# Optimization experiments

Hardware: AMD Instinct MI355X
Metric: run time of the kernel (lower is better)

Reference implementation:

```python
import jax, jax.numpy as jnp
import numpy as np

NBINS = 256  # tf.histogram_fixed_width(..., nbins=256)


def _colorspace():
    # tf.clip_by_value(tf.range(-1.0, 1.01, delta=1/127), -1, 1) -> 256 values
    cs = -1.0 + jnp.arange(NBINS, dtype=jnp.float32) / 127.0
    return jnp.clip(cs, -1.0, 1.0)


def _equalize_histogram(chan):
    # chan: (H, W) float32 in [-1, 1]
    h, w = chan.shape
    v = jnp.clip(chan.ravel(), -1.0, 1.0)
    idx = jnp.clip(((v + 1.0) * (NBINS / 2.0)).astype(jnp.int32), 0, NBINS - 1)
    hist = jnp.zeros(NBINS, jnp.int32).at[idx].add(1)
    cdf = jnp.cumsum(hist)
    cdf_min = jnp.min(cdf)
    pix_cnt = float(h * w)
    return (cdf - cdf_min).astype(jnp.float32) * 2.0 / (pix_cnt - 1.0) - 1.0


def _interpolate(dx, dy, x):
    # dx, dy: (K,) ; x: (N,) -> (N,) piecewise-linear interp via nearest-bin argmin
    delvals = jnp.abs(dx[None, :] - x[:, None])  # (N, K) big intermediate, as in TF
    ind1 = jnp.argmin(delvals, axis=1)
    ind0 = jnp.maximum(ind1 - 1, 0)
    x0, x1 = dx[ind0], dx[ind1]
    y0, y1 = dy[ind0], dy[ind1]
    denom = x1 - x0
    safe = jnp.where(denom == 0.0, 1.0, denom)  # guard flat-CDF degenerate bins
    interp = y0 + (y1 - y0) * (x - x0) / safe
    return jnp.where(x <= dx[0], dy[0], jnp.where(x >= dx[-1], dy[-1], interp))


def setup_inputs() -> dict:
    key = jax.random.key(0)
    k1, k2 = jax.random.split(key)
    H, W = 1024, 1024
    src = jax.random.uniform(k1, (H, W, 3), jnp.float32, minval=-1.0, maxval=1.0)
    tgt = jax.random.uniform(k2, (H, W, 3), jnp.float32, minval=-1.0, maxval=1.0)
    return {"src": src, "tgt": tgt}


def reference(src, tgt):
    h, w, _ = src.shape
    cs = _colorspace()
    res = []
    for i in range(3):
        s = src[:, :, i]
        t = tgt[:, :, i]
        cdfsrc = _equalize_histogram(s)
        cdftgt = _equalize_histogram(t)
        pxmap = _interpolate(cdftgt, cs, cdfsrc)      # (256,) color map
        mapped = _interpolate(cs, pxmap, s.ravel())   # (H*W,) per-pixel lookup
        res.append(mapped.reshape(h, w))
    return jnp.stack(res, axis=2)
```

## Files before the change

### kernel.cpp

```cpp
#include <hip/hip_runtime.h>

#define NBINS 256
#define SLOT (6 * NBINS)

__device__ __forceinline__ float csv(int i) {
    float c = -1.0f + (float)i / 127.0f;
    return fminf(fmaxf(c, -1.0f), 1.0f);
}

__device__ __forceinline__ int binof(float v) {
    v = fminf(fmaxf(v, -1.0f), 1.0f);
    int b = (int)((v + 1.0f) * 128.0f);
    return min(max(b, 0), NBINS - 1);
}

__global__ __launch_bounds__(256) void hm_hist(const float* __restrict__ src,
                                               const float* __restrict__ tgt,
                                               int ngroups, int n,
                                               int* __restrict__ partials) {
    __shared__ int lh[SLOT];
    for (int i = threadIdx.x; i < SLOT; i += blockDim.x) lh[i] = 0;
    __syncthreads();

    const float4* __restrict__ s4 = (const float4*)src;
    const float4* __restrict__ t4 = (const float4*)tgt;
    const int stride = gridDim.x * blockDim.x;
    for (int g = blockIdx.x * blockDim.x + threadIdx.x; g < ngroups; g += stride) {
        int b = g * 3;
        float4 s0 = s4[b], s1 = s4[b + 1], s2 = s4[b + 2];
        float4 t0 = t4[b], t1 = t4[b + 1], t2 = t4[b + 2];
        atomicAdd(&lh[0 * NBINS + binof(s0.x)], 1);
        atomicAdd(&lh[1 * NBINS + binof(s0.y)], 1);
        atomicAdd(&lh[2 * NBINS + binof(s0.z)], 1);
        atomicAdd(&lh[0 * NBINS + binof(s0.w)], 1);
        atomicAdd(&lh[1 * NBINS + binof(s1.x)], 1);
        atomicAdd(&lh[2 * NBINS + binof(s1.y)], 1);
        atomicAdd(&lh[0 * NBINS + binof(s1.z)], 1);
        atomicAdd(&lh[1 * NBINS + binof(s1.w)], 1);
        atomicAdd(&lh[2 * NBINS + binof(s2.x)], 1);
        atomicAdd(&lh[0 * NBINS + binof(s2.y)], 1);
        atomicAdd(&lh[1 * NBINS + binof(s2.z)], 1);
        atomicAdd(&lh[2 * NBINS + binof(s2.w)], 1);

        atomicAdd(&lh[3 * NBINS + binof(t0.x)], 1);
        atomicAdd(&lh[4 * NBINS + binof(t0.y)], 1);
        atomicAdd(&lh[5 * NBINS + binof(t0.z)], 1);
        atomicAdd(&lh[3 * NBINS + binof(t0.w)], 1);
        atomicAdd(&lh[4 * NBINS + binof(t1.x)], 1);
        atomicAdd(&lh[5 * NBINS + binof(t1.y)], 1);
        atomicAdd(&lh[3 * NBINS + binof(t1.z)], 1);
        atomicAdd(&lh[4 * NBINS + binof(t1.w)], 1);
        atomicAdd(&lh[5 * NBINS + binof(t2.x)], 1);
        atomicAdd(&lh[3 * NBINS + binof(t2.y)], 1);
        atomicAdd(&lh[4 * NBINS + binof(t2.z)], 1);
        atomicAdd(&lh[5 * NBINS + binof(t2.w)], 1);
    }
    if (blockIdx.x == 0) {
        int base = ngroups * 12;
        int rem = n - base;
        if ((int)threadIdx.x < rem) {
            int j = base + threadIdx.x;
            int c = j % 3;
            atomicAdd(&lh[c * NBINS + binof(src[j])], 1);
            atomicAdd(&lh[(3 + c) * NBINS + binof(tgt[j])], 1);
        }
    }
    __syncthreads();

    int* dst = partials + blockIdx.x * SLOT;
    for (int i = threadIdx.x; i < SLOT; i += blockDim.x) dst[i] = lh[i];
}

__global__ void hm_reduce(int* __restrict__ partials) {
    int h = blockIdx.x >> 4;
    int k = blockIdx.x & 15;
    int t = threadIdx.x;
    int base = (k * 16) * SLOT + h * NBINS + t;
    int s = 0;
    #pragma unroll
    for (int j = 0; j < 16; j++) s += partials[base + j * SLOT];
    partials[base] = s;
}

__global__ __launch_bounds__(1024) void hm_tables(const int* __restrict__ partials,
                                                  int nslots, int step,
                                                  float pixcnt_m1,
                                                  float* __restrict__ pxmap) {
    const int c = blockIdx.x;
    const int t = threadIdx.x;
    const int grp = t >> 8;
    const int bin = t & 255;

    __shared__ int red[8][NBINS];
    __shared__ int ss[NBINS], st[NBINS];
    __shared__ float cdfs[NBINS], cdft[NBINS];

    int as = 0, at = 0;
    for (int b = grp; b < nslots; b += 4) {
        const int* p = partials + (b * step) * SLOT;
        as += p[c * NBINS + bin];
        at += p[(3 + c) * NBINS + bin];
    }
    red[grp][bin] = as;
    red[4 + grp][bin] = at;
    __syncthreads();

    if (t < NBINS) {
        ss[t] = red[0][t] + red[1][t] + red[2][t] + red[3][t];
        st[t] = red[4][t] + red[5][t] + red[6][t] + red[7][t];
    }
    __syncthreads();

    for (int off = 1; off < NBINS; off <<= 1) {
        int a = 0, b = 0;
        if (t < NBINS && t >= off) { a = ss[t - off]; b = st[t - off]; }
        __syncthreads();
        if (t < NBINS && t >= off) { ss[t] += a; st[t] += b; }
        __syncthreads();
    }

    if (t < NBINS) {
        int mins = ss[0];
        int mint = st[0];
        cdfs[t] = (float)(ss[t] - mins) * 2.0f / pixcnt_m1 - 1.0f;
        cdft[t] = (float)(st[t] - mint) * 2.0f / pixcnt_m1 - 1.0f;
    }
    __syncthreads();

    if (t < NBINS) {
        float x = cdfs[t];
        int ind1 = 0;
        float best = fabsf(cdft[0] - x);
        for (int i = 1; i < NBINS; i++) {
            float d = fabsf(cdft[i] - x);
            if (d < best) { best = d; ind1 = i; }
        }
        int ind0 = max(ind1 - 1, 0);
        float x0 = cdft[ind0], x1 = cdft[ind1];
        float y0 = csv(ind0),  y1 = csv(ind1);
        float denom = x1 - x0;
        float safe = (denom == 0.0f) ? 1.0f : denom;
        float interp = y0 + (y1 - y0) * (x - x0) / safe;

        float r;
        if (x <= cdft[0])              r = csv(0);
        else if (x >= cdft[NBINS - 1]) r = csv(NBINS - 1);
        else                           r = interp;

        pxmap[c * NBINS + t] = r;
    }
}

__device__ __forceinline__ float map_one(float x, const float* __restrict__ y,
                                         const float* __restrict__ cs) {
    if (x <= -1.0f) return y[0];
    if (x >= 1.0f)  return y[NBINS - 1];
    float kf = (x + 1.0f) * 127.0f;
    int k = (int)(kf + 0.5f);
    int lo = max(k - 1, 0);
    int hi = min(k + 1, NBINS - 1);
    int ind1 = lo;
    float best = fabsf(cs[lo] - x);
    for (int j = lo + 1; j <= hi; j++) {
        float d = fabsf(cs[j] - x);
        if (d < best) { best = d; ind1 = j; }
    }
    int ind0 = max(ind1 - 1, 0);
    float x0 = cs[ind0], x1 = cs[ind1];
    float y0 = y[ind0],  y1 = y[ind1];
    float denom = x1 - x0;
    float safe = (denom == 0.0f) ? 1.0f : denom;
    return y0 + (y1 - y0) * (x - x0) / safe;
}

__global__ __launch_bounds__(256) void hm_map(const float* __restrict__ src,
                                              const float* __restrict__ pxmap,
                                              float* __restrict__ out,
                                              int ngroups, int n) {
    __shared__ float pm[3 * NBINS];
    __shared__ float cs[NBINS];
    for (int i = threadIdx.x; i < 3 * NBINS; i += blockDim.x) pm[i] = pxmap[i];
    for (int i = threadIdx.x; i < NBINS; i += blockDim.x) cs[i] = csv(i);
    __syncthreads();

    const float4* __restrict__ s4 = (const float4*)src;
    float4* __restrict__ o4 = (float4*)out;
    const int stride = gridDim.x * blockDim.x;
    for (int g = blockIdx.x * blockDim.x + threadIdx.x; g < ngroups; g += stride) {
        int b = g * 3;
        float4 s0 = s4[b], s1 = s4[b + 1], s2 = s4[b + 2];
        float4 r0, r1, r2;
        r0.x = map_one(s0.x, &pm[0 * NBINS], cs);
        r0.y = map_one(s0.y, &pm[1 * NBINS], cs);
        r0.z = map_one(s0.z, &pm[2 * NBINS], cs);
        r0.w = map_one(s0.w, &pm[0 * NBINS], cs);
        r1.x = map_one(s1.x, &pm[1 * NBINS], cs);
        r1.y = map_one(s1.y, &pm[2 * NBINS], cs);
        r1.z = map_one(s1.z, &pm[0 * NBINS], cs);
        r1.w = map_one(s1.w, &pm[1 * NBINS], cs);
        r2.x = map_one(s2.x, &pm[2 * NBINS], cs);
        r2.y = map_one(s2.y, &pm[0 * NBINS], cs);
        r2.z = map_one(s2.z, &pm[1 * NBINS], cs);
        r2.w = map_one(s2.w, &pm[2 * NBINS], cs);
        o4[b] = r0; o4[b + 1] = r1; o4[b + 2] = r2;
    }
    if (blockIdx.x == 0) {
        int base = ngroups * 12;
        int rem = n - base;
        if ((int)threadIdx.x < rem) {
            int j = base + threadIdx.x;
            int c = j % 3;
            out[j] = map_one(src[j], &pm[c * NBINS], cs);
        }
    }
}

extern "C" void kernel_launch(void* const* d_in, const int* in_sizes, int n_in,
                              void* d_out, int out_size, void* d_ws, size_t ws_size,
                              hipStream_t stream) {
    const float* src = (const float*)d_in[0];
    const float* tgt = (const float*)d_in[1];
    float* out = (float*)d_out;

    const int n = in_sizes[0];
    const int ngroups = n / 12;
    const int pixcnt = n / 3;

    float* pxmap    = (float*)d_ws;
    int*   partials = (int*)((char*)d_ws + 4096);

    const int slot_bytes = SLOT * (int)sizeof(int);
    int NB = 256;
    int need = (ngroups + 255) / 256;
    if (need < 1) need = 1;
    if (NB > need) NB = need;
    if (ws_size >= 4096 + (size_t)slot_bytes) {
        size_t avail = (ws_size - 4096) / slot_bytes;
        if (avail < (size_t)NB) NB = (int)avail;
    } else {
        NB = 1;
    }

    hm_hist<<<NB, 256, 0, stream>>>(src, tgt, ngroups, n, partials);

    if (NB == 256) {
        hm_reduce<<<96, NBINS, 0, stream>>>(partials);
        hm_tables<<<3, 1024, 0, stream>>>(partials, 16, 16,
                                          (float)pixcnt - 1.0f, pxmap);
    } else {
        hm_tables<<<3, 1024, 0, stream>>>(partials, NB, 1,
                                          (float)pixcnt - 1.0f, pxmap);
    }

    int mblocks = (ngroups + 255) / 256;
    if (mblocks > 1024) mblocks = 1024;
    if (mblocks < 1) mblocks = 1;
    hm_map<<<mblocks, 256, 0, stream>>>(src, pxmap, out, ngroups, n);
}
```

Measured before the change: 93.52 us.

## Drop separate partial-reduce kernel and double histogram block count

Removes the hm_reduce kernel launch, so hm_tables now sums every per-block partial histogram directly with an unrolled strided loop. The histogram kernel grid grows from 256 to 512 blocks, giving more parallelism over the 3M-element inputs. This saves one kernel launch and a global round trip, but the three-block tables kernel now reads twice as many partials serially (512 slots per channel), which may lengthen that tail stage.

New measurement: 108.8 us. 1.16x slower.

```diff
diff --git a/kernel.cpp b/kernel.cpp
--- a/kernel.cpp
+++ b/kernel.cpp
@@ -71,19 +71,8 @@
     for (int i = threadIdx.x; i < SLOT; i += blockDim.x) dst[i] = lh[i];
 }
 
-__global__ void hm_reduce(int* __restrict__ partials) {
-    int h = blockIdx.x >> 4;
-    int k = blockIdx.x & 15;
-    int t = threadIdx.x;
-    int base = (k * 16) * SLOT + h * NBINS + t;
-    int s = 0;
-    #pragma unroll
-    for (int j = 0; j < 16; j++) s += partials[base + j * SLOT];
-    partials[base] = s;
-}
-
 __global__ __launch_bounds__(1024) void hm_tables(const int* __restrict__ partials,
-                                                  int nslots, int step,
+                                                  int nslots,
                                                   float pixcnt_m1,
                                                   float* __restrict__ pxmap) {
     const int c = blockIdx.x;
@@ -96,10 +85,13 @@
     __shared__ float cdfs[NBINS], cdft[NBINS];
 
     int as = 0, at = 0;
+    const int offS = c * NBINS + bin;
+    const int offT = (3 + c) * NBINS + bin;
+    #pragma unroll 8
     for (int b = grp; b < nslots; b += 4) {
-        const int* p = partials + (b * step) * SLOT;
-        as += p[c * NBINS + bin];
-        at += p[(3 + c) * NBINS + bin];
+        const int* p = partials + b * SLOT;
+        as += p[offS];
+        at += p[offT];
     }
     red[grp][bin] = as;
     red[4 + grp][bin] = at;
@@ -230,7 +222,7 @@
     int*   partials = (int*)((char*)d_ws + 4096);
 
     const int slot_bytes = SLOT * (int)sizeof(int);
-    int NB = 256;
+    int NB = 512;
     int need = (ngroups + 255) / 256;
     if (need < 1) need = 1;
     if (NB > need) NB = need;
@@ -243,14 +235,7 @@
 
     hm_hist<<<NB, 256, 0, stream>>>(src, tgt, ngroups, n, partials);
 
-    if (NB == 256) {
-        hm_reduce<<<96, NBINS, 0, stream>>>(partials);
-        hm_tables<<<3, 1024, 0, stream>>>(partials, 16, 16,
-                                          (float)pixcnt - 1.0f, pxmap);
-    } else {
-        hm_tables<<<3, 1024, 0, stream>>>(partials, NB, 1,
-                                          (float)pixcnt - 1.0f, pxmap);
-    }
+    hm_tables<<<3, 1024, 0, stream>>>(partials, NB, (float)pixcnt - 1.0f, pxmap);
 
     int mblocks = (ngroups + 255) / 256;
     if (mblocks > 1024) mblocks = 1024;
```

## Fuse histogram, table build and mapping into one cooperative kernel

Applied to the files above, without the earlier changes.

Replaces the four-kernel sequence (histogram, reduce, tables, map) with a single cooperative kernel that uses grid-wide syncs between phases. It launches 256 blocks of 1024 threads, and the per-block partial histograms are reduced directly by three blocks. The aim is to remove the kernel launch gaps and the separate reduce pass. In exchange it adds grid.sync overhead, and most blocks sit idle during the table phase. If the cooperative launch fails, the code falls back to the old multi-kernel path.

Measured after the change: 295.0 us. 3.15x slower.

```diff
diff --git a/kernel.cpp b/kernel.cpp
--- a/kernel.cpp
+++ b/kernel.cpp
@@ -1,7 +1,12 @@
 #include <hip/hip_runtime.h>
+#include <hip/hip_cooperative_groups.h>
+
+namespace cg = cooperative_groups;
 
 #define NBINS 256
 #define SLOT (6 * NBINS)
+#define FNB  256
+#define FTH  1024
 
 __device__ __forceinline__ float csv(int i) {
     float c = -1.0f + (float)i / 127.0f;
@@ -12,6 +17,214 @@
     v = fminf(fmaxf(v, -1.0f), 1.0f);
     int b = (int)((v + 1.0f) * 128.0f);
     return min(max(b, 0), NBINS - 1);
+}
+
+__device__ __forceinline__ float map_one(float x, const float* __restrict__ y,
+                                         const float* __restrict__ cs) {
+    if (x <= -1.0f) return y[0];
+    if (x >= 1.0f)  return y[NBINS - 1];
+    float kf = (x + 1.0f) * 127.0f;
+    int k = (int)(kf + 0.5f);
+    int lo = max(k - 1, 0);
+    int hi = min(k + 1, NBINS - 1);
+    int ind1 = lo;
+    float best = fabsf(cs[lo] - x);
+    for (int j = lo + 1; j <= hi; j++) {
+        float d = fabsf(cs[j] - x);
+        if (d < best) { best = d; ind1 = j; }
+    }
+    int ind0 = max(ind1 - 1, 0);
+    float x0 = cs[ind0], x1 = cs[ind1];
+    float y0 = y[ind0],  y1 = y[ind1];
+    float denom = x1 - x0;
+    float safe = (denom == 0.0f) ? 1.0f : denom;
+    return y0 + (y1 - y0) * (x - x0) / safe;
+}
+
+__global__ __launch_bounds__(FTH) void hm_fused(const float* __restrict__ src,
+                                                const float* __restrict__ tgt,
+                                                float* __restrict__ out,
+                                                int ngroups, int n,
+                                                float pixcnt_m1,
+                                                float* __restrict__ pxmap,
+                                                int* __restrict__ partials) {
+    cg::grid_group grid = cg::this_grid();
+
+    __shared__ int lh[8 * NBINS];
+    __shared__ int ss[NBINS], st[NBINS];
+    __shared__ float cdfs[NBINS], cdft[NBINS];
+    __shared__ float pm[3 * NBINS];
+    __shared__ float cstab[NBINS];
+
+    const int t = threadIdx.x;
+
+    for (int i = t; i < SLOT; i += FTH) lh[i] = 0;
+    __syncthreads();
+
+    const float4* __restrict__ s4 = (const float4*)src;
+    const float4* __restrict__ t4 = (const float4*)tgt;
+    const int stride = gridDim.x * blockDim.x;
+    for (int g = blockIdx.x * blockDim.x + t; g < ngroups; g += stride) {
+        int b = g * 3;
+        float4 s0 = s4[b], s1 = s4[b + 1], s2 = s4[b + 2];
+        float4 t0 = t4[b], t1 = t4[b + 1], t2 = t4[b + 2];
+        atomicAdd(&lh[0 * NBINS + binof(s0.x)], 1);
+        atomicAdd(&lh[1 * NBINS + binof(s0.y)], 1);
+        atomicAdd(&lh[2 * NBINS + binof(s0.z)], 1);
+        atomicAdd(&lh[0 * NBINS + binof(s0.w)], 1);
+        atomicAdd(&lh[1 * NBINS + binof(s1.x)], 1);
+        atomicAdd(&lh[2 * NBINS + binof(s1.y)], 1);
+        atomicAdd(&lh[0 * NBINS + binof(s1.z)], 1);
+        atomicAdd(&lh[1 * NBINS + binof(s1.w)], 1);
+        atomicAdd(&lh[2 * NBINS + binof(s2.x)], 1);
+        atomicAdd(&lh[0 * NBINS + binof(s2.y)], 1);
+        atomicAdd(&lh[1 * NBINS + binof(s2.z)], 1);
+        atomicAdd(&lh[2 * NBINS + binof(s2.w)], 1);
+
+        atomicAdd(&lh[3 * NBINS + binof(t0.x)], 1);
+        atomicAdd(&lh[4 * NBINS + binof(t0.y)], 1);
+        atomicAdd(&lh[5 * NBINS + binof(t0.z)], 1);
+        atomicAdd(&lh[3 * NBINS + binof(t0.w)], 1);
+        atomicAdd(&lh[4 * NBINS + binof(t1.x)], 1);
+        atomicAdd(&lh[5 * NBINS + binof(t1.y)], 1);
+        atomicAdd(&lh[3 * NBINS + binof(t1.z)], 1);
+        atomicAdd(&lh[4 * NBINS + binof(t1.w)], 1);
+        atomicAdd(&lh[5 * NBINS + binof(t2.x)], 1);
+        atomicAdd(&lh[3 * NBINS + binof(t2.y)], 1);
+        atomicAdd(&lh[4 * NBINS + binof(t2.z)], 1);
+        atomicAdd(&lh[5 * NBINS + binof(t2.w)], 1);
+    }
+    if (blockIdx.x == 0) {
+        int base = ngroups * 12;
+        int rem = n - base;
+        if (t < rem) {
+            int j = base + t;
+            int c = j % 3;
+            atomicAdd(&lh[c * NBINS + binof(src[j])], 1);
+            atomicAdd(&lh[(3 + c) * NBINS + binof(tgt[j])], 1);
+        }
+    }
+    __syncthreads();
+
+    {
+        int* dst = partials + blockIdx.x * SLOT;
+        for (int i = t; i < SLOT; i += FTH) dst[i] = lh[i];
+    }
+
+    __threadfence();
+    grid.sync();
+
+    if (blockIdx.x < 3) {
+        const int c = blockIdx.x;
+        const int grp = t >> 8;
+        const int bin = t & 255;
+
+        int as = 0, at = 0;
+        const int offS = c * NBINS + bin;
+        const int offT = (3 + c) * NBINS + bin;
+        #pragma unroll 8
+        for (int b = grp; b < FNB; b += 4) {
+            const int* p = partials + b * SLOT;
+            as += p[offS];
+            at += p[offT];
+        }
+        lh[grp * NBINS + bin] = as;
+        lh[(4 + grp) * NBINS + bin] = at;
+        __syncthreads();
+
+        if (t < NBINS) {
+            ss[t] = lh[0 * NBINS + t] + lh[1 * NBINS + t] + lh[2 * NBINS + t] + lh[3 * NBINS + t];
+        } else if (t < 2 * NBINS) {
+            int b = t - NBINS;
+            st[b] = lh[4 * NBINS + b] + lh[5 * NBINS + b] + lh[6 * NBINS + b] + lh[7 * NBINS + b];
+        }
+        __syncthreads();
+
+        for (int off = 1; off < NBINS; off <<= 1) {
+            int a = 0; bool act = false;
+            if (t < NBINS) {
+                if (t >= off) { a = ss[t - off]; act = true; }
+            } else if (t < 2 * NBINS) {
+                int b = t - NBINS;
+                if (b >= off) { a = st[b - off]; act = true; }
+            }
+            __syncthreads();
+            if (act) {
+                if (t < NBINS) ss[t] += a;
+                else st[t - NBINS] += a;
+            }
+            __syncthreads();
+        }
+
+        if (t < NBINS) {
+            int mins = ss[0];
+            cdfs[t] = (float)(ss[t] - mins) * 2.0f / pixcnt_m1 - 1.0f;
+        } else if (t < 2 * NBINS) {
+            int b = t - NBINS;
+            int mint = st[0];
+            cdft[b] = (float)(st[b] - mint) * 2.0f / pixcnt_m1 - 1.0f;
+        }
+        __syncthreads();
+
+        if (t < NBINS) {
+            float x = cdfs[t];
+            int ind1 = 0;
+            float best = fabsf(cdft[0] - x);
+            for (int i = 1; i < NBINS; i++) {
+                float d = fabsf(cdft[i] - x);
+                if (d < best) { best = d; ind1 = i; }
+            }
+            int ind0 = max(ind1 - 1, 0);
+            float x0 = cdft[ind0], x1 = cdft[ind1];
+            float y0 = csv(ind0),  y1 = csv(ind1);
+            float denom = x1 - x0;
+            float safe = (denom == 0.0f) ? 1.0f : denom;
+            float interp = y0 + (y1 - y0) * (x - x0) / safe;
+
+            float r;
+            if (x <= cdft[0])              r = csv(0);
+            else if (x >= cdft[NBINS - 1]) r = csv(NBINS - 1);
+            else                           r = interp;
+
+            pxmap[c * NBINS + t] = r;
+        }
+    }
+
+    __threadfence();
+    grid.sync();
+
+    for (int i = t; i < 3 * NBINS; i += FTH) pm[i] = pxmap[i];
+    for (int i = t; i < NBINS; i += FTH) cstab[i] = csv(i);
+    __syncthreads();
+
+    float4* __restrict__ o4 = (float4*)out;
+    for (int g = blockIdx.x * blockDim.x + t; g < ngroups; g += stride) {
+        int b = g * 3;
+        float4 s0 = s4[b], s1 = s4[b + 1], s2 = s4[b + 2];
+        float4 r0, r1, r2;
+        r0.x = map_one(s0.x, &pm[0 * NBINS], cstab);
+        r0.y = map_one(s0.y, &pm[1 * NBINS], cstab);
+        r0.z = map_one(s0.z, &pm[2 * NBINS], cstab);
+        r0.w = map_one(s0.w, &pm[0 * NBINS], cstab);
+        r1.x = map_one(s1.x, &pm[1 * NBINS], cstab);
+        r1.y = map_one(s1.y, &pm[2 * NBINS], cstab);
+        r1.z = map_one(s1.z, &pm[0 * NBINS], cstab);
+        r1.w = map_one(s1.w, &pm[1 * NBINS], cstab);
+        r2.x = map_one(s2.x, &pm[2 * NBINS], cstab);
+        r2.y = map_one(s2.y, &pm[0 * NBINS], cstab);
+        r2.z = map_one(s2.z, &pm[1 * NBINS], cstab);
+        r2.w = map_one(s2.w, &pm[2 * NBINS], cstab);
+        o4[b] = r0; o4[b + 1] = r1; o4[b + 2] = r2;
+    }
+    if (blockIdx.x == 0) {
+        int base = ngroups * 12;
+        int rem = n - base;
+        if (t < rem) {
+            int j = base + t;
+            int c = j % 3;
+            out[j] = map_one(src[j], &pm[c * NBINS], cstab);
+        }
+    }
 }
 
 __global__ __launch_bounds__(256) void hm_hist(const float* __restrict__ src,
@@ -41,7 +254,6 @@
         atomicAdd(&lh[0 * NBINS + binof(s2.y)], 1);
         atomicAdd(&lh[1 * NBINS + binof(s2.z)], 1);
         atomicAdd(&lh[2 * NBINS + binof(s2.w)], 1);
-
         atomicAdd(&lh[3 * NBINS + binof(t0.x)], 1);
         atomicAdd(&lh[4 * NBINS + binof(t0.y)], 1);
         atomicAdd(&lh[5 * NBINS + binof(t0.z)], 1);
@@ -149,28 +361,6 @@
 
         pxmap[c * NBINS + t] = r;
     }
-}
-
-__device__ __forceinline__ float map_one(float x, const float* __restrict__ y,
-                                         const float* __restrict__ cs) {
-    if (x <= -1.0f) return y[0];
-    if (x >= 1.0f)  return y[NBINS - 1];
-    float kf = (x + 1.0f) * 127.0f;
-    int k = (int)(kf + 0.5f);
-    int lo = max(k - 1, 0);
-    int hi = min(k + 1, NBINS - 1);
-    int ind1 = lo;
-    float best = fabsf(cs[lo] - x);
-    for (int j = lo + 1; j <= hi; j++) {
-        float d = fabsf(cs[j] - x);
-        if (d < best) { best = d; ind1 = j; }
-    }
-    int ind0 = max(ind1 - 1, 0);
-    float x0 = cs[ind0], x1 = cs[ind1];
-    float y0 = y[ind0],  y1 = y[ind1];
-    float denom = x1 - x0;
-    float safe = (denom == 0.0f) ? 1.0f : denom;
-    return y0 + (y1 - y0) * (x - x0) / safe;
 }
 
 __global__ __launch_bounds__(256) void hm_map(const float* __restrict__ src,
@@ -230,6 +420,23 @@
     int*   partials = (int*)((char*)d_ws + 4096);
 
     const int slot_bytes = SLOT * (int)sizeof(int);
+    float pixm1 = (float)pixcnt - 1.0f;
+
+    bool coop_ok = (ws_size >= 4096 + (size_t)FNB * slot_bytes) && (ngroups >= 1);
+    if (coop_ok) {
+        const float* a_src = src; const float* a_tgt = tgt; float* a_out = out;
+        int a_ng = ngroups; int a_n = n; float a_px = pixm1;
+        float* a_pm = pxmap; int* a_pt = partials;
+        void* kargs[] = {(void*)&a_src, (void*)&a_tgt, (void*)&a_out,
+                         (void*)&a_ng, (void*)&a_n, (void*)&a_px,
+                         (void*)&a_pm, (void*)&a_pt};
+        hipError_t e = hipLaunchCooperativeKernel((const void*)hm_fused,
+                                                  dim3(FNB), dim3(FTH),
+                                                  kargs, 0, stream);
+        if (e == hipSuccess) return;
+        (void)hipGetLastError();
+    }
+
     int NB = 256;
     int need = (ngroups + 255) / 256;
     if (need < 1) need = 1;
@@ -245,11 +452,9 @@
 
     if (NB == 256) {
         hm_reduce<<<96, NBINS, 0, stream>>>(partials);
-        hm_tables<<<3, 1024, 0, stream>>>(partials, 16, 16,
-                                          (float)pixcnt - 1.0f, pxmap);
+        hm_tables<<<3, 1024, 0, stream>>>(partials, 16, 16, pixm1, pxmap);
     } else {
-        hm_tables<<<3, 1024, 0, stream>>>(partials, NB, 1,
-                                          (float)pixcnt - 1.0f, pxmap);
+        hm_tables<<<3, 1024, 0, stream>>>(partials, NB, 1, pixm1, pxmap);
     }
 
     int mblocks = (ngroups + 255) / 256;
```
